# Kernel tuning notes

Hardware: AMD Instinct MI355X
Metric: run time of the kernel (lower is better)

The kernel has to match this reference:

```python
import jax, jax.numpy as jnp
import numpy as np


def _init_relative_position_index(window_size: int) -> np.ndarray:
    coords = np.stack(np.meshgrid(np.arange(window_size), np.arange(window_size), indexing='ij'))
    coords_flatten = coords.reshape(2, -1)  # [2, wh*ww]
    rel = coords_flatten[:, :, None] - coords_flatten[:, None, :]  # [2, N, N]
    rel = rel.transpose(1, 2, 0).copy()
    rel[:, :, 0] += window_size - 1
    rel[:, :, 1] += window_size - 1
    rel[:, :, 0] *= 2 * window_size - 1
    return rel.sum(-1)  # [N, N] int


def setup_inputs() -> dict:
    B_, N, C, H, WH, NW = 2048, 49, 512, 16, 7, 64
    key = jax.random.key(0)
    ks = jax.random.split(key, 6)
    x = jax.random.normal(ks[0], (B_, N, C), dtype=jnp.float32)
    qkv_w = jax.random.normal(ks[1], (3 * C, C), dtype=jnp.float32) * 0.02
    qkv_b = jax.random.normal(ks[2], (3 * C,), dtype=jnp.float32) * 0.02
    rp_bias_table = jax.random.normal(ks[3], ((2 * WH - 1) ** 2, H), dtype=jnp.float32) * 0.02
    out_w = jax.random.normal(ks[4], (C, C), dtype=jnp.float32) * 0.02
    out_b = jax.random.normal(ks[5], (C,), dtype=jnp.float32) * 0.02
    rp_index = jnp.asarray(_init_relative_position_index(WH), dtype=jnp.int32)
    mask = jnp.zeros((NW, N, N), dtype=jnp.float32)  # 0/-inf shifted-window mask
    return {"x": x, "qkv_w": qkv_w, "qkv_b": qkv_b, "rp_index": rp_index,
            "rp_bias_table": rp_bias_table, "out_w": out_w, "out_b": out_b,
            "mask": mask, "nw": NW}


def reference(x, qkv_w, qkv_b, rp_index, rp_bias_table, out_w, out_b, mask, nw):
    B_, N, C = x.shape
    h = rp_bias_table.shape[1]
    dh = C // h
    scale = float(dh) ** -0.5

    # QKV projection; weight layout is (h dh 3) x C per the module's note.
    qkv = x @ qkv_w.T + qkv_b                      # [B_, N, 3C]
    qkv = qkv.reshape(B_, N, h, dh, 3)             # [B_, N, h, dh, 3]
    q = qkv[..., 0].transpose(0, 2, 1, 3)          # [B_, h, N, dh]
    k = qkv[..., 1].transpose(0, 2, 1, 3)
    v = qkv[..., 2].transpose(0, 2, 1, 3)

    attn = jnp.einsum('bhnd,bhmd->bhnm', q * scale, k)  # [B_, h, N, N]

    # gather relative position bias: [N*N] -> [N, N, h] -> [h, N, N]
    pb = rp_bias_table[rp_index.reshape(-1)].reshape(N, N, h).transpose(2, 0, 1)
    # NOTE: original adds the bias TWICE (attn += pb; attn += pb[None]); replicate.
    attn = attn + pb[None]
    attn = attn + pb[None]

    nW = mask.shape[0]
    attn = attn.reshape(B_ // nW, nW, h, N, N) + mask[None, :, None]
    attn = attn.reshape(B_, h, N, N)
    attn = jax.nn.softmax(attn, axis=-1)
    # attn_drop = proj_drop = 0.0 -> dropout is identity

    out = jnp.einsum('bhnm,bhmd->bhnd', attn, v)   # [B_, h, N, dh]
    out = out.transpose(0, 2, 1, 3).reshape(B_, N, h * dh)
    out = out @ out_w.T + out_b
    return out
```

## Files before the change

kernel.cpp:

```cpp
#include <hip/hip_runtime.h>
#include <hip/hip_bf16.h>
#include <stdint.h>

typedef short s16x8 __attribute__((ext_vector_type(8)));
typedef float f32x4 __attribute__((ext_vector_type(4)));

#define H_ 16
#define DH 32
#define NTOK 49
#define CDIM 512
#define SCALE 0.17677669529663687f

typedef const __attribute__((address_space(1))) uint32_t* gas_ptr;
typedef __attribute__((address_space(3))) uint32_t* las_ptr;
#define GLL16(g, l) __builtin_amdgcn_global_load_lds((gas_ptr)(g), (las_ptr)(l), 16, 0, 0)

__device__ __forceinline__ short f2bf(float f){
  union { __bf16 h; short s; } u;
  u.h = (__bf16)f;
  return u.s;
}

__device__ __forceinline__ s16x8 pack8(float4 a, float4 b){
  s16x8 r;
  r[0]=f2bf(a.x); r[1]=f2bf(a.y); r[2]=f2bf(a.z); r[3]=f2bf(a.w);
  r[4]=f2bf(b.x); r[5]=f2bf(b.y); r[6]=f2bf(b.z); r[7]=f2bf(b.w);
  return r;
}

__device__ __forceinline__ int xcd_swz(int orig, int nwg){
  int q = nwg >> 3, r = nwg & 7;
  int x = orig & 7, idx = orig >> 3;
  return (x < r ? x*(q+1) : r*(q+1) + (x - r)*q) + idx;
}

__global__ void prep_wq_kernel(const float* __restrict__ w, const float* __restrict__ b,
                               short* __restrict__ wq, float* __restrict__ pb)
{
  int t = blockIdx.x*256 + threadIdx.x;
  int jp = t >> 6, kg = t & 63;
  int s = jp >> 9, h = (jp >> 5) & 15, d = jp & 31;
  int srow = h*96 + d*3 + s;
  float fac = (s == 0) ? SCALE : 1.0f;
  const float* wr = w + (size_t)srow*CDIM + kg*8;
  float4 a = *(const float4*)wr;
  float4 c = *(const float4*)(wr+4);
  a.x*=fac; a.y*=fac; a.z*=fac; a.w*=fac;
  c.x*=fac; c.y*=fac; c.z*=fac; c.w*=fac;
  ((s16x8*)(wq + (size_t)jp*CDIM))[kg] = pack8(a,c);
  if (kg == 0) pb[jp] = b[srow]*fac;
}

__global__ void prep_wo_kernel(const float* __restrict__ w, short* __restrict__ wo)
{
  int t = blockIdx.x*256 + threadIdx.x;
  int j = t >> 6, kg = t & 63;
  const float* wr = w + (size_t)j*CDIM + kg*8;
  float4 a = *(const float4*)wr;
  float4 c = *(const float4*)(wr+4);
  ((s16x8*)(wo + (size_t)j*CDIM))[kg] = pack8(a,c);
}

__global__ void prep_bm_kernel(const int* __restrict__ idx, const float* __restrict__ tab,
                               const float* __restrict__ mask, float* __restrict__ bm)
{
  int wh = blockIdx.x;
  int w = wh >> 4, h = wh & 15;
  const float* mw = mask + (size_t)w*2401;
  float* o = bm + (size_t)wh*2401;
  for (int i = threadIdx.x; i < 2401; i += 256)
    o[i] = mw[i] + 2.0f*tab[idx[i]*H_ + h];
}

__global__ void cvt_kernel(const float* __restrict__ src, short* __restrict__ dst, int n8)
{
  int i = blockIdx.x*blockDim.x + threadIdx.x;
  int stride = gridDim.x*blockDim.x;
  for (; i < n8; i += stride){
    float4 a = ((const float4*)src)[2*i];
    float4 b = ((const float4*)src)[2*i+1];
    ((s16x8*)dst)[i] = pack8(a,b);
  }
}

template<int EPI>
__global__ __launch_bounds__(256)
void gemm128(const short* __restrict__ A, const short* __restrict__ Bm,
             const float* __restrict__ pb,
             short* __restrict__ Q, short* __restrict__ Kd, short* __restrict__ V,
             float* __restrict__ outF, int ntiles, int nwg, int b0)
{
  __shared__ __align__(16) short As[2][8192];
  __shared__ __align__(16) short Bs[2][8192];
  const int tid = threadIdx.x, w = tid >> 6, l = tid & 63;
  const int wg = xcd_swz(blockIdx.x, nwg);
  const int mt = wg / ntiles, jt = wg % ntiles;
  const int wr = w >> 1, wc = w & 1, lg = l >> 4, lc = l & 15;

  const int srow = w*8 + (l >> 3);
  const int sbyte = ((l & 7) ^ (l >> 3)) << 4;
  const char* gA = (const char*)A  + ((size_t)(mt*128 + srow))*1024 + sbyte;
  const char* gB = (const char*)Bm + ((size_t)(jt*128 + srow))*1024 + sbyte;

  f32x4 acc[4][4];
  #pragma unroll
  for (int i=0;i<4;++i)
    #pragma unroll
    for (int j=0;j<4;++j) acc[i][j] = (f32x4){0.f,0.f,0.f,0.f};

  #pragma unroll
  for (int i=0;i<4;++i){
    GLL16(gA + i*32768, (char*)As[0] + i*4096 + w*1024);
    GLL16(gB + i*32768, (char*)Bs[0] + i*4096 + w*1024);
  }
  __syncthreads();

  int buf = 0;
  for (int kt=0; kt<8; ++kt){
    if (kt < 7){
      const char* ga2 = gA + (kt+1)*128;
      const char* gb2 = gB + (kt+1)*128;
      #pragma unroll
      for (int i=0;i<4;++i){
        GLL16(ga2 + i*32768, (char*)As[buf^1] + i*4096 + w*1024);
        GLL16(gb2 + i*32768, (char*)Bs[buf^1] + i*4096 + w*1024);
      }
    }
    const char* pA = (const char*)As[buf];
    const char* pB = (const char*)Bs[buf];
    #pragma unroll
    for (int kk=0; kk<2; ++kk){
      const int kbyte = (kk*64 + lg*16) ^ ((lc & 7) << 4);
      s16x8 af[4], bf_[4];
      #pragma unroll
      for (int i=0;i<4;++i)
        af[i]  = *(const s16x8*)(pA + (wr*64 + i*16 + lc)*128 + kbyte);
      #pragma unroll
      for (int j=0;j<4;++j)
        bf_[j] = *(const s16x8*)(pB + (wc*64 + j*16 + lc)*128 + kbyte);
      __builtin_amdgcn_s_setprio(1);
      #pragma unroll
      for (int i=0;i<4;++i)
        #pragma unroll
        for (int j=0;j<4;++j)
          acc[i][j] = __builtin_amdgcn_mfma_f32_16x16x32_bf16(af[i], bf_[j], acc[i][j], 0,0,0);
      __builtin_amdgcn_s_setprio(0);
    }
    __syncthreads();
    buf ^= 1;
  }

  const int cb = jt*128 + wc*64;
  if (EPI == 0){
    const int s_sel = cb >> 9;
    short* dst = (s_sel==0) ? Q : (s_sel==1 ? Kd : V);
    float bv[4]; int hj[4], dj[4];
    #pragma unroll
    for (int j=0;j<4;++j){
      int cc = cb + j*16 + lc;
      bv[j] = pb[cc];
      hj[j] = (cc >> 5) & 15;
      dj[j] = cc & 31;
    }
    #pragma unroll
    for (int i=0;i<4;++i){
      #pragma unroll
      for (int r=0;r<4;++r){
        int grow = mt*128 + wr*64 + i*16 + lg*4 + r;
        int bl = grow / 49;
        int n  = grow - bl*49;
        #pragma unroll
        for (int j=0;j<4;++j)
          dst[(((size_t)bl*H_ + hj[j])*NTOK + n)*DH + dj[j]] = f2bf(acc[i][j][r] + bv[j]);
      }
    }
  } else {
    float bv[4];
    #pragma unroll
    for (int j=0;j<4;++j) bv[j] = pb[cb + j*16 + lc];
    #pragma unroll
    for (int i=0;i<4;++i){
      #pragma unroll
      for (int r=0;r<4;++r){
        int grow = mt*128 + wr*64 + i*16 + lg*4 + r;
        size_t o = ((size_t)(b0*NTOK) + grow)*CDIM + cb;
        #pragma unroll
        for (int j=0;j<4;++j)
          outF[o + j*16 + lc] = acc[i][j][r] + bv[j];
      }
    }
  }
}

__global__ __launch_bounds__(256)
void attn_kernel(const short* __restrict__ Q, const short* __restrict__ Kt,
                 const short* __restrict__ V, const float* __restrict__ bm,
                 short* __restrict__ AO, int b0, int nW)
{
  __shared__ __align__(16) short P[4][64][72];
  const int tid = threadIdx.x, wv = tid >> 6, lane = tid & 63;
  const int lg = lane >> 4, lc = lane & 15;
  const int pair = blockIdx.x*4 + wv;
  const int bl = pair >> 4, h = pair & 15;
  const short* q = Q  + ((size_t)bl*H_ + h)*NTOK*DH;
  const short* k = Kt + ((size_t)bl*H_ + h)*NTOK*DH;
  const short* v = V  + ((size_t)bl*H_ + h)*NTOK*DH;

  s16x8 qa[4], kb[4];
  #pragma unroll
  for (int t=0;t<4;++t){
    int r = t*16 + lc; if (r > 48) r = 48;
    qa[t] = *(const s16x8*)(q + r*DH + lg*8);
    kb[t] = *(const s16x8*)(k + r*DH + lg*8);
  }
  f32x4 S[4][4];
  #pragma unroll
  for (int i=0;i<4;++i)
    #pragma unroll
    for (int j=0;j<4;++j) S[i][j] = (f32x4){0.f,0.f,0.f,0.f};
  #pragma unroll
  for (int i=0;i<4;++i)
    #pragma unroll
    for (int j=0;j<4;++j)
      S[i][j] = __builtin_amdgcn_mfma_f32_16x16x32_bf16(qa[i], kb[j], S[i][j], 0,0,0);

  const int widx = (b0 + bl) % nW;
  const float* bmh = bm + ((size_t)widx*H_ + h)*2401;

  float rinv[4][4];
  #pragma unroll
  for (int i=0;i<4;++i){
    #pragma unroll
    for (int r=0;r<4;++r){
      int row = i*16 + lg*4 + r;
      float mx = -3.0e38f;
      #pragma unroll
      for (int j=0;j<4;++j){
        int col = j*16 + lc;
        float sv = S[i][j][r];
        if (row < 49 && col < 49) sv += bmh[row*49+col];
        else sv = -1.0e30f;
        S[i][j][r] = sv;
        mx = fmaxf(mx, sv);
      }
      #pragma unroll
      for (int off=1; off<16; off<<=1) mx = fmaxf(mx, __shfl_xor(mx, off, 64));
      float sum = 0.f;
      #pragma unroll
      for (int j=0;j<4;++j){
        float e = __expf(S[i][j][r] - mx);
        S[i][j][r] = e;
        sum += e;
      }
      #pragma unroll
      for (int off=1; off<16; off<<=1) sum += __shfl_xor(sum, off, 64);
      rinv[i][r] = 1.0f / sum;
    }
  }

  #pragma unroll
  for (int i=0;i<4;++i)
    #pragma unroll
    for (int j=0;j<4;++j)
      #pragma unroll
      for (int r=0;r<4;++r)
        P[wv][i*16 + lg*4 + r][j*16 + lc] = f2bf(S[i][j][r]);

  s16x8 vb[2][2];
  #pragma unroll
  for (int kt=0;kt<2;++kt)
    #pragma unroll
    for (int nt=0;nt<2;++nt){
      s16x8 t;
      #pragma unroll
      for (int e=0;e<8;++e){
        int kk = kt*32 + lg*8 + e; if (kk > 48) kk = 48;
        t[e] = v[kk*DH + nt*16 + lc];
      }
      vb[kt][nt] = t;
    }
  f32x4 O[4][2];
  #pragma unroll
  for (int i=0;i<4;++i){ O[i][0] = (f32x4){0.f,0.f,0.f,0.f}; O[i][1] = (f32x4){0.f,0.f,0.f,0.f}; }
  #pragma unroll
  for (int i=0;i<4;++i){
    #pragma unroll
    for (int kt=0;kt<2;++kt){
      s16x8 pa = *(const s16x8*)&P[wv][i*16 + lc][kt*32 + lg*8];
      #pragma unroll
      for (int nt=0;nt<2;++nt)
        O[i][nt] = __builtin_amdgcn_mfma_f32_16x16x32_bf16(pa, vb[kt][nt], O[i][nt], 0,0,0);
    }
  }
  #pragma unroll
  for (int i=0;i<4;++i)
    #pragma unroll
    for (int r=0;r<4;++r){
      int row = i*16 + lg*4 + r;
      if (row < 49){
        size_t o = ((size_t)bl*NTOK + row)*CDIM + h*DH;
        float rv = rinv[i][r];
        AO[o + lc]      = f2bf(O[i][0][r]*rv);
        AO[o + 16 + lc] = f2bf(O[i][1][r]*rv);
      }
    }
}

extern "C" void kernel_launch(void* const* d_in, const int* in_sizes, int n_in,
                              void* d_out, int out_size, void* d_ws, size_t ws_size,
                              hipStream_t stream)
{
  const float* x      = (const float*)d_in[0];
  const float* qkv_w  = (const float*)d_in[1];
  const float* qkv_b  = (const float*)d_in[2];
  const int*   rp_idx = (const int*)d_in[3];
  const float* rp_tab = (const float*)d_in[4];
  const float* out_w  = (const float*)d_in[5];
  const float* out_b  = (const float*)d_in[6];
  const float* mask   = (const float*)d_in[7];
  const int nW = in_sizes[7] / (NTOK*NTOK);
  float* out = (float*)d_out;

  char* base = (char*)d_ws;
  size_t off = 0;
  auto alloc = [&](size_t bytes)->char*{
    char* p = base + off;
    off = (off + bytes + 255) & ~(size_t)255;
    return p;
  };
  float* bm  = (float*)alloc((size_t)nW*H_*2401*4);
  short* wq  = (short*)alloc((size_t)1536*CDIM*2);
  float* pbq = (float*)alloc(1536*4);
  short* wo  = (short*)alloc((size_t)CDIM*CDIM*2);

  int CB = 512;
  while (CB > 128){
    size_t need = off + 5*(size_t)CB*50176;
    if (need <= ws_size) break;
    CB >>= 1;
  }
  short* xb = (short*)alloc((size_t)CB*50176);
  short* Q  = (short*)alloc((size_t)CB*50176);
  short* K  = (short*)alloc((size_t)CB*50176);
  short* V  = (short*)alloc((size_t)CB*50176);
  short* AO = (short*)alloc((size_t)CB*50176);

  hipLaunchKernelGGL(prep_bm_kernel, dim3(nW*H_), dim3(256), 0, stream,
                     rp_idx, rp_tab, mask, bm);
  hipLaunchKernelGGL(prep_wq_kernel, dim3(1536*64/256), dim3(256), 0, stream,
                     qkv_w, qkv_b, wq, pbq);
  hipLaunchKernelGGL(prep_wo_kernel, dim3(512*64/256), dim3(256), 0, stream,
                     out_w, wo);

  const int nchunk = 2048 / CB;
  const int mtiles = CB*NTOK/128;
  const int n8 = CB*3136;
  for (int c=0; c<nchunk; ++c){
    int b0 = c*CB;
    hipLaunchKernelGGL(cvt_kernel, dim3(2048), dim3(256), 0, stream,
                       x + (size_t)b0*NTOK*CDIM, xb, n8);
    hipLaunchKernelGGL((gemm128<0>), dim3(mtiles*12), dim3(256), 0, stream,
                       xb, wq, pbq, Q, K, V, (float*)nullptr, 12, mtiles*12, b0);
    hipLaunchKernelGGL(attn_kernel, dim3(CB*4), dim3(256), 0, stream,
                       Q, K, V, bm, AO, b0, nW);
    hipLaunchKernelGGL((gemm128<1>), dim3(mtiles*4), dim3(256), 0, stream,
                       AO, wo, out_b, (short*)nullptr, (short*)nullptr, (short*)nullptr,
                       out, 4, mtiles*4, b0);
  }
}
```

Measured before the change: 575.9 us.

## Group attention blocks by window/head and stage bias-mask slab in LDS

Attention blocks are now indexed so that all four waves in a block share the same window index and head. The combined bias+mask slab is then loaded cooperatively into shared memory once per block instead of each lane gathering it from global memory. The bias table is repadded to a 50-float row stride and a 2464-float slab so it can be copied with aligned float4 loads. The chunk size is raised to 1024 to reduce launches, which costs more workspace and adds a __syncthreads per block.

```diff
diff --git a/kernel.cpp b/kernel.cpp
--- a/kernel.cpp
+++ b/kernel.cpp
@@ -61,15 +61,19 @@
   ((s16x8*)(wo + (size_t)j*CDIM))[kg] = pack8(a,c);
 }
 
+#define BMSTR 50
+#define BMSLAB 2464
 __global__ void prep_bm_kernel(const int* __restrict__ idx, const float* __restrict__ tab,
                                const float* __restrict__ mask, float* __restrict__ bm)
 {
   int wh = blockIdx.x;
   int w = wh >> 4, h = wh & 15;
   const float* mw = mask + (size_t)w*2401;
-  float* o = bm + (size_t)wh*2401;
-  for (int i = threadIdx.x; i < 2401; i += 256)
-    o[i] = mw[i] + 2.0f*tab[idx[i]*H_ + h];
+  float* o = bm + (size_t)wh*BMSLAB;
+  for (int i = threadIdx.x; i < 2401; i += 256){
+    int r = i / 49, c = i - r*49;
+    o[r*BMSTR + c] = mw[i] + 2.0f*tab[idx[i]*H_ + h];
+  }
 }
 
 __global__ void cvt_kernel(const float* __restrict__ src, short* __restrict__ dst, int n8)
@@ -192,19 +196,40 @@
   }
 }
 
+template<int GROUPED>
 __global__ __launch_bounds__(256)
 void attn_kernel(const short* __restrict__ Q, const short* __restrict__ Kt,
                  const short* __restrict__ V, const float* __restrict__ bm,
                  short* __restrict__ AO, int b0, int nW)
 {
   __shared__ __align__(16) short P[4][64][72];
+  __shared__ __align__(16) float bmL[BMSLAB];
   const int tid = threadIdx.x, wv = tid >> 6, lane = tid & 63;
   const int lg = lane >> 4, lc = lane & 15;
-  const int pair = blockIdx.x*4 + wv;
-  const int bl = pair >> 4, h = pair & 15;
+  const int h = blockIdx.x & 15, rest = blockIdx.x >> 4;
+
+  int bl, widx;
+  if (GROUPED){
+    widx = rest % nW;
+    int g4 = rest / nW;
+    bl = widx + (g4*4 + wv)*nW;
+  } else {
+    bl = rest*4 + wv;
+    widx = (b0 + bl) % nW;
+  }
+
   const short* q = Q  + ((size_t)bl*H_ + h)*NTOK*DH;
   const short* k = Kt + ((size_t)bl*H_ + h)*NTOK*DH;
   const short* v = V  + ((size_t)bl*H_ + h)*NTOK*DH;
+
+  if (GROUPED){
+    const float4* bmg = (const float4*)(bm + ((size_t)widx*H_ + h)*BMSLAB);
+    #pragma unroll
+    for (int i=0;i<3;++i){
+      int s = tid + i*256;
+      if (s < BMSLAB/4) ((float4*)bmL)[s] = bmg[s];
+    }
+  }
 
   s16x8 qa[4], kb[4];
   #pragma unroll
@@ -224,8 +249,8 @@
     for (int j=0;j<4;++j)
       S[i][j] = __builtin_amdgcn_mfma_f32_16x16x32_bf16(qa[i], kb[j], S[i][j], 0,0,0);
 
-  const int widx = (b0 + bl) % nW;
-  const float* bmh = bm + ((size_t)widx*H_ + h)*2401;
+  if (GROUPED) __syncthreads();
+  const float* bmh = GROUPED ? bmL : (bm + ((size_t)widx*H_ + h)*BMSLAB);
 
   float rinv[4][4];
   #pragma unroll
@@ -238,7 +263,7 @@
       for (int j=0;j<4;++j){
         int col = j*16 + lc;
         float sv = S[i][j][r];
-        if (row < 49 && col < 49) sv += bmh[row*49+col];
+        if (row < 49 && col < 49) sv += bmh[row*BMSTR+col];
         else sv = -1.0e30f;
         S[i][j][r] = sv;
         mx = fmaxf(mx, sv);
@@ -328,12 +353,12 @@
     off = (off + bytes + 255) & ~(size_t)255;
     return p;
   };
-  float* bm  = (float*)alloc((size_t)nW*H_*2401*4);
+  float* bm  = (float*)alloc((size_t)nW*H_*BMSLAB*4);
   short* wq  = (short*)alloc((size_t)1536*CDIM*2);
   float* pbq = (float*)alloc(1536*4);
   short* wo  = (short*)alloc((size_t)CDIM*CDIM*2);
 
-  int CB = 512;
+  int CB = 1024;
   while (CB > 128){
     size_t need = off + 5*(size_t)CB*50176;
     if (need <= ws_size) break;
@@ -352,6 +377,7 @@
   hipLaunchKernelGGL(prep_wo_kernel, dim3(512*64/256), dim3(256), 0, stream,
                      out_w, wo);
 
+  const bool grouped = (CB % (4*nW)) == 0;
   const int nchunk = 2048 / CB;
   const int mtiles = CB*NTOK/128;
   const int n8 = CB*3136;
@@ -361,8 +387,12 @@
                        x + (size_t)b0*NTOK*CDIM, xb, n8);
     hipLaunchKernelGGL((gemm128<0>), dim3(mtiles*12), dim3(256), 0, stream,
                        xb, wq, pbq, Q, K, V, (float*)nullptr, 12, mtiles*12, b0);
-    hipLaunchKernelGGL(attn_kernel, dim3(CB*4), dim3(256), 0, stream,
-                       Q, K, V, bm, AO, b0, nW);
+    if (grouped)
+      hipLaunchKernelGGL((attn_kernel<1>), dim3(CB*4), dim3(256), 0, stream,
+                         Q, K, V, bm, AO, b0, nW);
+    else
+      hipLaunchKernelGGL((attn_kernel<0>), dim3(CB*4), dim3(256), 0, stream,
+                         Q, K, V, bm, AO, b0, nW);
     hipLaunchKernelGGL((gemm128<1>), dim3(mtiles*4), dim3(256), 0, stream,
                        AO, wo, out_b, (short*)nullptr, (short*)nullptr, (short*)nullptr,
                        out, 4, mtiles*4, b0);
```

Measured after the change: 582.3 us. About the same (+1.1%).
